# Optimization experiments

Hardware: AMD Instinct MI355X
Metric: run time of the kernel (lower is better)

Reference implementation:

```python
import jax, jax.numpy as jnp
import numpy as np

N = 100000
E = 1600000
NEG_SLOPE_ATTN = 0.2   # DGL GATConv default negative_slope
NEG_SLOPE_ACT = 0.01   # F.leaky_relu default


def gat_conv(x, src, dst, W, al, ar, b):
    """DGL-style GATConv with a single head.
    x: [N, Fin]; W: [Fin, H*Fout]; al, ar: [H, Fout]; b: [H*Fout].
    Returns [N, H, Fout]."""
    H, Fout = al.shape
    h = (x @ W).reshape(-1, H, Fout)                 # [N,H,Fout]
    el = jnp.sum(h * al, axis=-1)                    # [N,H]
    er = jnp.sum(h * ar, axis=-1)                    # [N,H]
    e = jax.nn.leaky_relu(el[src] + er[dst], NEG_SLOPE_ATTN)  # [E,H]
    # edge softmax over incoming edges of each dst node
    m = jax.ops.segment_max(e, dst, num_segments=N)  # [N,H]
    ex = jnp.exp(e - m[dst])                         # [E,H]
    denom = jax.ops.segment_sum(ex, dst, num_segments=N)      # [N,H]
    a = ex / denom[dst]                              # [E,H]
    msg = h[src] * a[:, :, None]                     # [E,H,Fout]
    out = jax.ops.segment_sum(msg, dst, num_segments=N)       # [N,H,Fout]
    return out + b.reshape(1, H, Fout)


def setup_inputs() -> dict:
    key = jax.random.key(0)
    ks = jax.random.split(key, 16)
    features = jax.random.normal(ks[0], (N, 3), dtype=jnp.float32)
    src = jax.random.randint(ks[1], (E,), 0, N)
    dst = jax.random.randint(ks[2], (E,), 0, N)

    def glorot(k, shape):
        fan = shape[0] + shape[-1]
        s = jnp.sqrt(2.0 / fan).astype(jnp.float32)
        return jax.random.normal(k, shape, dtype=jnp.float32) * s

    W1 = glorot(ks[3], (3, 64));   al1 = glorot(ks[4], (1, 64));  ar1 = glorot(ks[5], (1, 64));  b1 = jnp.zeros((64,), jnp.float32)
    W2 = glorot(ks[6], (64, 64));  al2 = glorot(ks[7], (1, 64));  ar2 = glorot(ks[8], (1, 64));  b2 = jnp.zeros((64,), jnp.float32)
    W3 = glorot(ks[9], (64, 3));   al3 = glorot(ks[10], (1, 3));  ar3 = glorot(ks[11], (1, 3));  b3 = jnp.zeros((3,), jnp.float32)
    return {"features": features, "src": src, "dst": dst,
            "W1": W1, "al1": al1, "ar1": ar1, "b1": b1,
            "W2": W2, "al2": al2, "ar2": ar2, "b2": b2,
            "W3": W3, "al3": al3, "ar3": ar3, "b3": b3}


def reference(features, src, dst, W1, al1, ar1, b1, W2, al2, ar2, b2, W3, al3, ar3, b3):
    x = gat_conv(features, src, dst, W1, al1, ar1, b1)      # [N,1,64]
    x = jax.nn.leaky_relu(x, NEG_SLOPE_ACT)
    x = gat_conv(x[:, 0, :], src, dst, W2, al2, ar2, b2)     # [N,1,64]
    x = jax.nn.leaky_relu(x, NEG_SLOPE_ACT)
    x = gat_conv(x[:, 0, :], src, dst, W3, al3, ar3, b3)     # [N,1,3]
    return x[:, 0, :]                                        # [N,3]
```

## Files before the change

kernel.cpp:

```cpp
#include <hip/hip_runtime.h>
#include <hip/hip_fp16.h>
#include <math.h>


#define NEG_BIG (-1e30f)
#define SORT_CAP 6144
#define BSTRIDE 6144
#define CHUNK 8192

__device__ inline float waveSum(float v) {
#pragma unroll
  for (int off = 32; off; off >>= 1) v += __shfl_xor(v, off, 64);
  return v;
}

__device__ inline float halfSum(float v) {
#pragma unroll
  for (int off = 16; off; off >>= 1) v += __shfl_xor(v, off, 64);
  return v;
}

__device__ inline float halfMax(float v) {
#pragma unroll
  for (int off = 16; off; off >>= 1) v = fmaxf(v, __shfl_xor(v, off, 64));
  return v;
}

__device__ inline int waveMaxI(int v) {
#pragma unroll
  for (int off = 32; off; off >>= 1) v = max(v, __shfl_xor(v, off, 64));
  return v;
}

__device__ inline int rlI(int v, int l) { return __builtin_amdgcn_readlane(v, l); }
__device__ inline float rlF(float v, int l) {
  return __int_as_float(__builtin_amdgcn_readlane(__float_as_int(v), l));
}
__device__ inline int ntI(const int* p) { return __builtin_nontemporal_load(p); }

__global__ __launch_bounds__(1024) void k_bin(
    const int* __restrict__ src, const int* __restrict__ dst,
    int* __restrict__ gcursor, unsigned* __restrict__ binned, int E, int NBK) {
  __shared__ int lcnt[512];
  __shared__ int lbase[512];
  int tid = threadIdx.x;
  for (int b = tid; b < NBK; b += 1024) lcnt[b] = 0;
  __syncthreads();
  int e0 = blockIdx.x * CHUNK;
  int e1 = min(e0 + CHUNK, E);
  for (int e = e0 + tid; e < e1; e += 1024)
    atomicAdd(&lcnt[ntI(&dst[e]) >> 8], 1);
  __syncthreads();
  for (int b = tid; b < NBK; b += 1024) {
    int c = lcnt[b];
    lbase[b] = c ? atomicAdd(&gcursor[b], c) : 0;
    lcnt[b] = 0;
  }
  __syncthreads();
  for (int e = e0 + tid; e < e1; e += 1024) {
    int dd = ntI(&dst[e]);
    int ss = ntI(&src[e]);
    int b = dd >> 8;
    int pos = lbase[b] + atomicAdd(&lcnt[b], 1);
    if (pos < BSTRIDE)
      binned[(size_t)b * BSTRIDE + pos] =
          ((unsigned)(dd & 255) << 24) | (unsigned)ss;
  }
}

__global__ void k_bscan(const int* __restrict__ cnt, int* __restrict__ base,
                        int NBK, int E, int* __restrict__ startv, int N) {
  __shared__ int s[1024];
  int t = threadIdx.x;
  int v = (t < NBK) ? cnt[t] : 0;
  s[t] = v;
  __syncthreads();
  for (int off = 1; off < 1024; off <<= 1) {
    int u = (t >= off) ? s[t - off] : 0;
    __syncthreads();
    s[t] += u;
    __syncthreads();
  }
  int excl = s[t] - v;
  if (t <= NBK) base[t] = excl;
  if (t == 0) startv[N] = E;
}

__global__ __launch_bounds__(256) void k_sort(
    const unsigned* __restrict__ binned, const int* __restrict__ base,
    int* __restrict__ csr, int* __restrict__ startv, int N) {
  __shared__ unsigned sbuf[SORT_CAP];
  __shared__ unsigned obuf[SORT_CAP];
  __shared__ int hist[256];
  __shared__ int scn[256];
  __shared__ int cur[256];
  int b = blockIdx.x;
  int tid = threadIdx.x;
  int gbase = base[b];
  int cnt = min(base[b + 1] - gbase, BSTRIDE);
  const unsigned* bsrc = binned + (size_t)b * BSTRIDE;
  hist[tid] = 0;
  __syncthreads();
  if (cnt <= SORT_CAP) {
    for (int i = tid; i < cnt; i += 256) {
      unsigned w = bsrc[i];
      sbuf[i] = w;
      atomicAdd(&hist[w >> 24], 1);
    }
    __syncthreads();
    int v = hist[tid];
    scn[tid] = v;
    __syncthreads();
    for (int off = 1; off < 256; off <<= 1) {
      int u = (tid >= off) ? scn[tid - off] : 0;
      __syncthreads();
      scn[tid] += u;
      __syncthreads();
    }
    int excl = scn[tid] - v;
    cur[tid] = excl;
    int dn = b * 256 + tid;
    if (dn < N) startv[dn] = gbase + excl;
    __syncthreads();
    for (int i = tid; i < cnt; i += 256) {
      unsigned w = sbuf[i];
      int p = atomicAdd(&cur[w >> 24], 1);
      obuf[p] = w & 0xFFFFFFu;
    }
    __syncthreads();
    for (int i = tid; i < cnt; i += 256) csr[gbase + i] = (int)obuf[i];
  } else {
    for (int i = tid; i < cnt; i += 256)
      atomicAdd(&hist[bsrc[i] >> 24], 1);
    __syncthreads();
    int v = hist[tid];
    scn[tid] = v;
    __syncthreads();
    for (int off = 1; off < 256; off <<= 1) {
      int u = (tid >= off) ? scn[tid - off] : 0;
      __syncthreads();
      scn[tid] += u;
      __syncthreads();
    }
    int excl = scn[tid] - v;
    cur[tid] = excl;
    int dn = b * 256 + tid;
    if (dn < N) startv[dn] = gbase + excl;
    __syncthreads();
    for (int i = tid; i < cnt; i += 256) {
      unsigned w = bsrc[i];
      int p = atomicAdd(&cur[w >> 24], 1);
      csr[gbase + p] = (int)(w & 0xFFFFFFu);
    }
  }
}

__global__ void k_prep(const float* __restrict__ W1, const float* __restrict__ al1,
                       const float* __restrict__ ar1, const float* __restrict__ W2,
                       const float* __restrict__ al2, const float* __restrict__ ar2,
                       float* __restrict__ uvw) {
  int lane = threadIdx.x & 63;
  float a = al1[lane], r = ar1[lane];
#pragma unroll
  for (int i = 0; i < 3; ++i) {
    float w = W1[i * 64 + lane];
    float ui = waveSum(w * a);
    float vi = waveSum(w * r);
    if (lane == 0) { uvw[i] = ui; uvw[3 + i] = vi; }
  }
  float sa = 0.f, sr = 0.f;
  for (int j = 0; j < 64; ++j) {
    float w = W2[lane * 64 + j];
    sa = fmaf(w, al2[j], sa);
    sr = fmaf(w, ar2[j], sr);
  }
  uvw[8 + lane] = sa;
  uvw[72 + lane] = sr;
}

__global__ void k_padx(const float* __restrict__ x, const float* __restrict__ uvw,
                       float4* __restrict__ x4, float* __restrict__ er1, int N) {
  int n = blockIdx.x * blockDim.x + threadIdx.x;
  if (n >= N) return;
  float x0 = __builtin_nontemporal_load(&x[n * 3]);
  float x1 = __builtin_nontemporal_load(&x[n * 3 + 1]);
  float x2 = __builtin_nontemporal_load(&x[n * 3 + 2]);
  float el = fmaf(x0, uvw[0], fmaf(x1, uvw[1], x2 * uvw[2]));
  float er = fmaf(x0, uvw[3], fmaf(x1, uvw[4], x2 * uvw[5]));
  x4[n] = make_float4(x0, x1, x2, el);
  er1[n] = er;
}

__global__ __launch_bounds__(256) void k_agg1x(
    const float4* __restrict__ x4, const float* __restrict__ er1,
    const float* __restrict__ W1, const float* __restrict__ b1,
    const float* __restrict__ uvw, const int* __restrict__ start,
    const int* __restrict__ csr, float4* __restrict__ a4,
    float* __restrict__ er2, int N) {
  int tid = threadIdx.x;
  int wave = tid >> 6, lane = tid & 63, hl = lane & 31, half = lane >> 5;
  int pA = blockIdx.x * 8 + wave * 2;
  int pn = pA + half;
  int n = (pn < N) ? pn : 0;
  int beg = start[n], end = start[n + 1];
  float ern = er1[n];
  float m = NEG_BIG, d = 0.f, X0 = 0.f, X1 = 0.f, X2 = 0.f;
  for (int base = beg; base < end; base += 32) {
    int idx = base + hl;
    int s = (idx < end) ? ntI(&csr[idx]) : 0;
    s = ((unsigned)s < (unsigned)N) ? s : 0;
    float4 hv = x4[s];
    float e = hv.w + ern;
    e = e > 0.f ? e : 0.2f * e;
    e = (idx < end) ? e : NEG_BIG;
    float mn = fmaxf(m, halfMax(e));
    float sc = __expf(m - mn);
    float q = __expf(e - mn);
    d = d * sc + halfSum(q);
    X0 = X0 * sc + halfSum(q * hv.x);
    X1 = X1 * sc + halfSum(q * hv.y);
    X2 = X2 * sc + halfSum(q * hv.z);
    m = mn;
  }
  float inv = (end > beg) ? 1.f / d : 0.f;
  X0 *= inv; X1 *= inv; X2 *= inv;
  float A0 = rlF(X0, 0), A1 = rlF(X1, 0), A2 = rlF(X2, 0);
  float B0 = rlF(X0, 32), B1 = rlF(X1, 32), B2 = rlF(X2, 32);
  float w1a = W1[lane], w1b = W1[64 + lane], w1c = W1[128 + lane];
  float bb = b1[lane];
  float vA = fmaf(A0, w1a, fmaf(A1, w1b, fmaf(A2, w1c, bb)));
  vA = vA > 0.f ? vA : 0.01f * vA;
  float vB = fmaf(B0, w1a, fmaf(B1, w1b, fmaf(B2, w1c, bb)));
  vB = vB > 0.f ? vB : 0.01f * vB;
  float wal = uvw[8 + lane], war = uvw[72 + lane];
  float eA = waveSum(vA * wal);
  float rA = waveSum(vA * war);
  float eB = waveSum(vB * wal);
  float rB = waveSum(vB * war);
  if (lane == 0) {
    if (pA < N) { a4[pA] = make_float4(A0, A1, A2, eA); er2[pA] = rA; }
    int pB = pA + 1;
    if (pB < N) { a4[pB] = make_float4(B0, B1, B2, eB); er2[pB] = rB; }
  }
}

__global__ __launch_bounds__(256) void k_agg2r(
    const float4* __restrict__ a4, const float* __restrict__ er2,
    const int* __restrict__ start, const int* __restrict__ csr,
    const float* __restrict__ W1, const float* __restrict__ b1,
    __half* __restrict__ xa, int N) {
  __shared__ float4 sAV[4][64];
  int tid = threadIdx.x;
  int wave = tid >> 6, lane = tid & 63, hl = lane & 31, half = lane >> 5;
  int pn = blockIdx.x * 8 + wave * 2 + half;
  int n = (pn < N) ? pn : 0;
  int beg = start[n], end = start[n + 1];
  int deg = end - beg;
  int maxd = __builtin_amdgcn_readfirstlane(waveMaxI(deg));
  float ern = er2[n];
  int k0 = 2 * hl;
  float wa0 = W1[k0],     wb0 = W1[64 + k0],     wc0 = W1[128 + k0],     bb0 = b1[k0];
  float wa1 = W1[k0 + 1], wb1 = W1[64 + k0 + 1], wc1 = W1[128 + k0 + 1], bb1 = b1[k0 + 1];
  float acc0 = 0.f, acc1 = 0.f;

  float aA = 0.f, v0s = 0.f, v1s = 0.f, v2s = 0.f;
  if (maxd <= 32) {
    int idx = beg + hl;
    int s = (idx < end) ? ntI(&csr[idx]) : 0;
    s = ((unsigned)s < (unsigned)N) ? s : 0;
    float4 av = a4[s];
    float e = av.w + ern;
    e = e > 0.f ? e : 0.2f * e;
    e = (idx < end) ? e : NEG_BIG;
    float mm = halfMax(e);
    float q = __expf(e - mm);
    float dsum = halfSum(q);
    float inv = (deg > 0) ? 1.f / dsum : 0.f;
    aA = q * inv;
    v0s = av.x; v1s = av.y; v2s = av.z;
  }
  sAV[wave][half * 32 + hl] = make_float4(aA, v0s, v1s, v2s);
  __syncthreads();

  if (maxd <= 32) {
    const float4* sp = &sAV[wave][half * 32];
    for (int j = 0; j < maxd; j += 4) {
#pragma unroll
      for (int k = 0; k < 4; ++k) {
        float4 w = sp[j + k];
        float a = w.x;
        float v0 = fmaf(w.w, wc0, fmaf(w.z, wb0, fmaf(w.y, wa0, bb0)));
        v0 = v0 > 0.f ? v0 : 0.01f * v0;
        float v1 = fmaf(w.w, wc1, fmaf(w.z, wb1, fmaf(w.y, wa1, bb1)));
        v1 = v1 > 0.f ? v1 : 0.01f * v1;
        acc0 = fmaf(a, v0, acc0);
        acc1 = fmaf(a, v1, acc1);
      }
    }
  } else {
    float m = NEG_BIG, dsum = 0.f;
    for (int base = beg; base < end; base += 32) {
      int idx = base + hl;
      int s = (idx < end) ? csr[idx] : 0;
      s = ((unsigned)s < (unsigned)N) ? s : 0;
      float e = a4[s].w + ern;
      e = e > 0.f ? e : 0.2f * e;
      e = (idx < end) ? e : NEG_BIG;
      float mn = fmaxf(m, halfMax(e));
      dsum = dsum * __expf(m - mn) + halfSum(__expf(e - mn));
      m = mn;
    }
    float inv = (deg > 0) ? 1.f / dsum : 0.f;
    for (int base = beg; base < end; base += 32) {
      int idx = base + hl;
      int s = (idx < end) ? csr[idx] : 0;
      s = ((unsigned)s < (unsigned)N) ? s : 0;
      float e = a4[s].w + ern;
      e = e > 0.f ? e : 0.2f * e;
      float a = (idx < end) ? __expf(e - m) * inv : 0.f;
      for (int j = 0; j < 32; ++j) {
        int sAx = rlI(s, j), sBx = rlI(s, j + 32);
        float aAx = rlF(a, j), aBx = rlF(a, j + 32);
        int sj = half ? sBx : sAx;
        float aj = half ? aBx : aAx;
        float4 av = a4[sj];
        float v0 = fmaf(av.z, wc0, fmaf(av.y, wb0, fmaf(av.x, wa0, bb0)));
        v0 = v0 > 0.f ? v0 : 0.01f * v0;
        float v1 = fmaf(av.z, wc1, fmaf(av.y, wb1, fmaf(av.x, wa1, bb1)));
        v1 = v1 > 0.f ? v1 : 0.01f * v1;
        acc0 = fmaf(aj, v0, acc0);
        acc1 = fmaf(aj, v1, acc1);
      }
    }
  }
  if (pn < N) {
    __half2 hv = __float22half2_rn(make_float2(acc0, acc1));
    ((__half2*)xa)[(size_t)pn * 32 + hl] = hv;
  }
}

__global__ __launch_bounds__(256) void k_gemm3(
    const __half* xa_in, const float* __restrict__ W2,
    const float* __restrict__ b2, const float* __restrict__ W3,
    const float* __restrict__ al3, float* __restrict__ h3, int N) {
  __shared__ float sW[64 * 64];
  __shared__ float sX[64 * 64];
  __shared__ float sW3[192];
  int tid = threadIdx.x;
  for (int i = tid; i < 4096; i += 256) sW[i] = W2[i];
  if (tid < 192) sW3[tid] = W3[tid];
  const unsigned* xu = (const unsigned*)xa_in;
  size_t base = (size_t)blockIdx.x * 2048;
  size_t limit = (size_t)N * 32;
  for (int i = tid; i < 2048; i += 256) {
    size_t gi = base + i;
    unsigned u = (gi < limit) ? __builtin_nontemporal_load(&xu[gi]) : 0u;
    __half2 hh = *(__half2*)&u;
    float2 f = __half22float2(hh);
    sX[2 * i] = f.x;
    sX[2 * i + 1] = f.y;
  }
  __syncthreads();
  int wave = tid >> 6, f = tid & 63;
  int r0 = wave * 16;
  float acc[16];
#pragma unroll
  for (int i = 0; i < 16; ++i) acc[i] = 0.f;
  const float2* sX2 = (const float2*)sX;
  for (int k2 = 0; k2 < 32; ++k2) {
    float wv0 = sW[(2 * k2) * 64 + f];
    float wv1 = sW[(2 * k2 + 1) * 64 + f];
#pragma unroll
    for (int i = 0; i < 16; ++i) {
      float2 xv = sX2[(r0 + i) * 32 + k2];
      acc[i] = fmaf(xv.x, wv0, fmaf(xv.y, wv1, acc[i]));
    }
  }
  float bf = b2[f];
  __syncthreads();
#pragma unroll
  for (int i = 0; i < 16; ++i) {
    float r = acc[i] + bf;
    r = r > 0.f ? r : 0.01f * r;
    sX[(r0 + i) * 64 + f] = r;
  }
  __syncthreads();
  int row = tid >> 2, j = tid & 3;
  int j3 = (j < 3) ? j : 0;
  float p = 0.f;
  for (int i = 0; i < 64; ++i) {
    int ff = (row + i) & 63;
    p = fmaf(sX[row * 64 + ff], sW3[ff * 3 + j3], p);
  }
  int lb = (tid & 63) & ~3;
  float q0 = __shfl(p, lb + 0, 64);
  float q1 = __shfl(p, lb + 1, 64);
  float q2 = __shfl(p, lb + 2, 64);
  float val = (j < 3) ? p : fmaf(q0, al3[0], fmaf(q1, al3[1], q2 * al3[2]));
  int grow = blockIdx.x * 64 + row;
  if (grow < N) h3[(size_t)blockIdx.x * 256 + tid] = val;
}

__global__ __launch_bounds__(256) void k_agg3(
    const float4* __restrict__ h3, const int* __restrict__ start,
    const int* __restrict__ csr, const float* __restrict__ ar3,
    const float* __restrict__ b, float* __restrict__ out, int N) {
  int tid = threadIdx.x;
  int wave = tid >> 6, lane = tid & 63, hl = lane & 31, half = lane >> 5;
  int pn = blockIdx.x * 8 + wave * 2 + half;
  int n = (pn < N) ? pn : 0;
  int beg = start[n], end = start[n + 1];
  float4 hn = h3[n];
  float ern = fmaf(hn.x, ar3[0], fmaf(hn.y, ar3[1], hn.z * ar3[2]));
  float m = NEG_BIG, d = 0.f, Q0 = 0.f, Q1 = 0.f, Q2 = 0.f;
  for (int base = beg; base < end; base += 32) {
    int idx = base + hl;
    int s = (idx < end) ? ntI(&csr[idx]) : 0;
    s = ((unsigned)s < (unsigned)N) ? s : 0;
    float4 hv = h3[s];
    float e = hv.w + ern;
    e = e > 0.f ? e : 0.2f * e;
    e = (idx < end) ? e : NEG_BIG;
    float mn = fmaxf(m, halfMax(e));
    float sc = __expf(m - mn);
    float q = __expf(e - mn);
    d = d * sc + halfSum(q);
    Q0 = Q0 * sc + halfSum(q * hv.x);
    Q1 = Q1 * sc + halfSum(q * hv.y);
    Q2 = Q2 * sc + halfSum(q * hv.z);
    m = mn;
  }
  float inv = (end > beg) ? 1.f / d : 0.f;
  if (hl == 0 && pn < N) {
    out[n * 3 + 0] = fmaf(Q0, inv, b[0]);
    out[n * 3 + 1] = fmaf(Q1, inv, b[1]);
    out[n * 3 + 2] = fmaf(Q2, inv, b[2]);
  }
}

extern "C" void kernel_launch(void* const* d_in, const int* in_sizes, int n_in,
                              void* d_out, int out_size, void* d_ws, size_t ws_size,
                              hipStream_t stream) {
  const int N = in_sizes[0] / 3;
  const int E = in_sizes[1];
  const float* feats = (const float*)d_in[0];
  const int* src = (const int*)d_in[1];
  const int* dst = (const int*)d_in[2];
  const float* W1  = (const float*)d_in[3];
  const float* al1 = (const float*)d_in[4];
  const float* ar1 = (const float*)d_in[5];
  const float* b1  = (const float*)d_in[6];
  const float* W2  = (const float*)d_in[7];
  const float* al2 = (const float*)d_in[8];
  const float* ar2 = (const float*)d_in[9];
  const float* b2  = (const float*)d_in[10];
  const float* W3  = (const float*)d_in[11];
  const float* al3 = (const float*)d_in[12];
  const float* ar3 = (const float*)d_in[13];
  const float* b3  = (const float*)d_in[14];

  const int NBK = (N + 255) >> 8;

  char* ws = (char*)d_ws;
  size_t off = 0;
  auto alloc = [&](size_t bytes) -> void* {
    void* p = ws + off;
    off = (off + bytes + 255) & ~(size_t)255;
    return p;
  };
  int* startv  = (int*)alloc((size_t)(N + 1) * 4);
  int* csr     = (int*)alloc((size_t)E * 4);
  float* er2v  = (float*)alloc((size_t)N * 4);
  float* er1   = (float*)alloc((size_t)N * 4);
  int* gcount  = (int*)alloc((size_t)NBK * 4);
  int* baseb   = (int*)alloc((size_t)(NBK + 1) * 4);
  float* uvw   = (float*)alloc(1024);
  float* h3    = (float*)alloc((size_t)N * 4 * 4);
  float4* x4   = (float4*)alloc((size_t)N * 16);
  float4* a4   = (float4*)alloc((size_t)N * 16);
  __half* xa   = (__half*)alloc((size_t)N * 64 * 2);
  unsigned* binned = (unsigned*)xa;

  const int NB  = (N + 255) / 256;
  const int NB8 = (N + 7) / 8;
  const int GB  = (N + 63) / 64;
  const int CB  = (E + CHUNK - 1) / CHUNK;

  k_prep<<<1, 64, 0, stream>>>(W1, al1, ar1, W2, al2, ar2, uvw);
  k_padx<<<NB, 256, 0, stream>>>(feats, uvw, x4, er1, N);

  hipMemsetAsync(gcount, 0, (size_t)NBK * 4, stream);
  k_bin<<<CB, 1024, 0, stream>>>(src, dst, gcount, binned, E, NBK);
  k_bscan<<<1, 1024, 0, stream>>>(gcount, baseb, NBK, E, startv, N);
  k_sort<<<NBK, 256, 0, stream>>>(binned, baseb, csr, startv, N);

  k_agg1x<<<NB8, 256, 0, stream>>>(x4, er1, W1, b1, uvw, startv, csr,
                                   a4, er2v, N);
  k_agg2r<<<NB8, 256, 0, stream>>>(a4, er2v, startv, csr, W1, b1, xa, N);
  k_gemm3<<<GB, 256, 0, stream>>>(xa, W2, b2, W3, al3, h3, N);
  k_agg3<<<NB8, 256, 0, stream>>>((const float4*)h3, startv, csr, ar3, b3,
                                  (float*)d_out, N);
}
```

Measured before the change: 243.6 us.

## Switch layer-1 and layer-3 aggregation to one thread per node with prefetch

The k_agg1x and k_agg3 kernels previously used a half-wave of 32 lanes per destination node, with shuffle reductions on every edge batch. They now give each node its own thread, which walks its edges serially with an online softmax and prefetches source features two edges ahead. In k_agg1x the 64-wide projection and attention dot products become a per-thread loop over weights staged in shared memory. With average degree near 16, most lanes in the old scheme sat idle, so this removes that waste and the shuffle cost. In exchange, each thread's gathers are serial and uncoalesced, threads in a wave do unequal work when degrees differ, and the per-thread 64-iteration loop adds ALU work.

```diff
diff --git a/kernel.cpp b/kernel.cpp
--- a/kernel.cpp
+++ b/kernel.cpp
@@ -197,51 +197,58 @@
     const float* __restrict__ uvw, const int* __restrict__ start,
     const int* __restrict__ csr, float4* __restrict__ a4,
     float* __restrict__ er2, int N) {
+  __shared__ float4 sWp[64];
+  __shared__ float2 sLR[64];
   int tid = threadIdx.x;
-  int wave = tid >> 6, lane = tid & 63, hl = lane & 31, half = lane >> 5;
-  int pA = blockIdx.x * 8 + wave * 2;
-  int pn = pA + half;
-  int n = (pn < N) ? pn : 0;
+  if (tid < 64) {
+    sWp[tid] = make_float4(W1[tid], W1[64 + tid], W1[128 + tid], b1[tid]);
+    sLR[tid] = make_float2(uvw[8 + tid], uvw[72 + tid]);
+  }
+  __syncthreads();
+  int n = blockIdx.x * 256 + tid;
+  if (n >= N) return;
   int beg = start[n], end = start[n + 1];
   float ern = er1[n];
   float m = NEG_BIG, d = 0.f, X0 = 0.f, X1 = 0.f, X2 = 0.f;
-  for (int base = beg; base < end; base += 32) {
-    int idx = base + hl;
-    int s = (idx < end) ? ntI(&csr[idx]) : 0;
-    s = ((unsigned)s < (unsigned)N) ? s : 0;
-    float4 hv = x4[s];
+  int ia = beg, ib = beg + 1;
+  int s0 = (ia < end) ? ntI(&csr[ia]) : 0;
+  s0 = ((unsigned)s0 < (unsigned)N) ? s0 : 0;
+  float4 h0 = x4[s0];
+  int s1 = (ib < end) ? ntI(&csr[ib]) : 0;
+  s1 = ((unsigned)s1 < (unsigned)N) ? s1 : 0;
+  float4 h1 = x4[s1];
+  for (int i = beg; i < end; ++i) {
+    float4 hv = h0;
+    h0 = h1;
+    int ip = i + 2;
+    int sp = (ip < end) ? ntI(&csr[ip]) : 0;
+    sp = ((unsigned)sp < (unsigned)N) ? sp : 0;
+    h1 = x4[sp];
     float e = hv.w + ern;
     e = e > 0.f ? e : 0.2f * e;
-    e = (idx < end) ? e : NEG_BIG;
-    float mn = fmaxf(m, halfMax(e));
+    float mn = fmaxf(m, e);
     float sc = __expf(m - mn);
     float q = __expf(e - mn);
-    d = d * sc + halfSum(q);
-    X0 = X0 * sc + halfSum(q * hv.x);
-    X1 = X1 * sc + halfSum(q * hv.y);
-    X2 = X2 * sc + halfSum(q * hv.z);
+    d = fmaf(d, sc, q);
+    X0 = fmaf(X0, sc, q * hv.x);
+    X1 = fmaf(X1, sc, q * hv.y);
+    X2 = fmaf(X2, sc, q * hv.z);
     m = mn;
   }
   float inv = (end > beg) ? 1.f / d : 0.f;
-  X0 *= inv; X1 *= inv; X2 *= inv;
-  float A0 = rlF(X0, 0), A1 = rlF(X1, 0), A2 = rlF(X2, 0);
-  float B0 = rlF(X0, 32), B1 = rlF(X1, 32), B2 = rlF(X2, 32);
-  float w1a = W1[lane], w1b = W1[64 + lane], w1c = W1[128 + lane];
-  float bb = b1[lane];
-  float vA = fmaf(A0, w1a, fmaf(A1, w1b, fmaf(A2, w1c, bb)));
-  vA = vA > 0.f ? vA : 0.01f * vA;
-  float vB = fmaf(B0, w1a, fmaf(B1, w1b, fmaf(B2, w1c, bb)));
-  vB = vB > 0.f ? vB : 0.01f * vB;
-  float wal = uvw[8 + lane], war = uvw[72 + lane];
-  float eA = waveSum(vA * wal);
-  float rA = waveSum(vA * war);
-  float eB = waveSum(vB * wal);
-  float rB = waveSum(vB * war);
-  if (lane == 0) {
-    if (pA < N) { a4[pA] = make_float4(A0, A1, A2, eA); er2[pA] = rA; }
-    int pB = pA + 1;
-    if (pB < N) { a4[pB] = make_float4(B0, B1, B2, eB); er2[pB] = rB; }
-  }
+  float A0 = X0 * inv, A1 = X1 * inv, A2 = X2 * inv;
+  float el = 0.f, er = 0.f;
+#pragma unroll 4
+  for (int k = 0; k < 64; ++k) {
+    float4 w = sWp[k];
+    float v = fmaf(A2, w.z, fmaf(A1, w.y, fmaf(A0, w.x, w.w)));
+    v = v > 0.f ? v : 0.01f * v;
+    float2 lr = sLR[k];
+    el = fmaf(v, lr.x, el);
+    er = fmaf(v, lr.y, er);
+  }
+  a4[n] = make_float4(A0, A1, A2, el);
+  er2[n] = er;
 }
 
 __global__ __launch_bounds__(256) void k_agg2r(
@@ -405,37 +412,41 @@
     const float4* __restrict__ h3, const int* __restrict__ start,
     const int* __restrict__ csr, const float* __restrict__ ar3,
     const float* __restrict__ b, float* __restrict__ out, int N) {
-  int tid = threadIdx.x;
-  int wave = tid >> 6, lane = tid & 63, hl = lane & 31, half = lane >> 5;
-  int pn = blockIdx.x * 8 + wave * 2 + half;
-  int n = (pn < N) ? pn : 0;
+  int n = blockIdx.x * 256 + threadIdx.x;
+  if (n >= N) return;
   int beg = start[n], end = start[n + 1];
   float4 hn = h3[n];
   float ern = fmaf(hn.x, ar3[0], fmaf(hn.y, ar3[1], hn.z * ar3[2]));
   float m = NEG_BIG, d = 0.f, Q0 = 0.f, Q1 = 0.f, Q2 = 0.f;
-  for (int base = beg; base < end; base += 32) {
-    int idx = base + hl;
-    int s = (idx < end) ? ntI(&csr[idx]) : 0;
-    s = ((unsigned)s < (unsigned)N) ? s : 0;
-    float4 hv = h3[s];
+  int ia = beg, ib = beg + 1;
+  int s0 = (ia < end) ? ntI(&csr[ia]) : 0;
+  s0 = ((unsigned)s0 < (unsigned)N) ? s0 : 0;
+  float4 h0 = h3[s0];
+  int s1 = (ib < end) ? ntI(&csr[ib]) : 0;
+  s1 = ((unsigned)s1 < (unsigned)N) ? s1 : 0;
+  float4 h1 = h3[s1];
+  for (int i = beg; i < end; ++i) {
+    float4 hv = h0;
+    h0 = h1;
+    int ip = i + 2;
+    int sp = (ip < end) ? ntI(&csr[ip]) : 0;
+    sp = ((unsigned)sp < (unsigned)N) ? sp : 0;
+    h1 = h3[sp];
     float e = hv.w + ern;
     e = e > 0.f ? e : 0.2f * e;
-    e = (idx < end) ? e : NEG_BIG;
-    float mn = fmaxf(m, halfMax(e));
+    float mn = fmaxf(m, e);
     float sc = __expf(m - mn);
     float q = __expf(e - mn);
-    d = d * sc + halfSum(q);
-    Q0 = Q0 * sc + halfSum(q * hv.x);
-    Q1 = Q1 * sc + halfSum(q * hv.y);
-    Q2 = Q2 * sc + halfSum(q * hv.z);
+    d = fmaf(d, sc, q);
+    Q0 = fmaf(Q0, sc, q * hv.x);
+    Q1 = fmaf(Q1, sc, q * hv.y);
+    Q2 = fmaf(Q2, sc, q * hv.z);
     m = mn;
   }
   float inv = (end > beg) ? 1.f / d : 0.f;
-  if (hl == 0 && pn < N) {
-    out[n * 3 + 0] = fmaf(Q0, inv, b[0]);
-    out[n * 3 + 1] = fmaf(Q1, inv, b[1]);
-    out[n * 3 + 2] = fmaf(Q2, inv, b[2]);
-  }
+  out[n * 3 + 0] = fmaf(Q0, inv, b[0]);
+  out[n * 3 + 1] = fmaf(Q1, inv, b[1]);
+  out[n * 3 + 2] = fmaf(Q2, inv, b[2]);
 }
 
 extern "C" void kernel_launch(void* const* d_in, const int* in_sizes, int n_in,
@@ -494,10 +505,10 @@
   k_bscan<<<1, 1024, 0, stream>>>(gcount, baseb, NBK, E, startv, N);
   k_sort<<<NBK, 256, 0, stream>>>(binned, baseb, csr, startv, N);
 
-  k_agg1x<<<NB8, 256, 0, stream>>>(x4, er1, W1, b1, uvw, startv, csr,
-                                   a4, er2v, N);
+  k_agg1x<<<NB, 256, 0, stream>>>(x4, er1, W1, b1, uvw, startv, csr,
+                                  a4, er2v, N);
   k_agg2r<<<NB8, 256, 0, stream>>>(a4, er2v, startv, csr, W1, b1, xa, N);
   k_gemm3<<<GB, 256, 0, stream>>>(xa, W2, b2, W3, al3, h3, N);
-  k_agg3<<<NB8, 256, 0, stream>>>((const float4*)h3, startv, csr, ar3, b3,
-                                  (float*)d_out, N);
-}
+  k_agg3<<<NB, 256, 0, stream>>>((const float4*)h3, startv, csr, ar3, b3,
+                                 (float*)d_out, N);
+}
```

After: 248.5 us. +2.0%, slower.
